# Performance work log

Hardware: AMD Instinct MI355X
Metric: run time of the kernel (lower is better)

The kernel has to match this reference:

```python
import jax, jax.numpy as jnp
import numpy as np

N, M, D = 60000, 96, 16  # voxels, centroids, descriptor_dim
NB = 4                    # batches (scenes)


def setup_inputs() -> dict:
    key = jax.random.key(0)
    ks = jax.random.split(key, 10)
    voxel_desc = jax.random.normal(ks[0], (N, D), jnp.float32)
    centroid_conf = jax.random.uniform(ks[1], (M, 1), jnp.float32)
    offsets = jax.random.normal(ks[2], (N, 3), jnp.float32)
    # 1x1 Conv2d weights act as plain linears over the channel dim
    c_in = 2 * D + 7          # 39
    c_hid = D + 3             # 19
    W1 = jax.random.normal(ks[3], (c_hid, c_in), jnp.float32) / np.sqrt(c_in)
    b1 = jax.random.normal(ks[4], (c_hid,), jnp.float32) * 0.01
    W2 = jax.random.normal(ks[5], (1, c_hid), jnp.float32) / np.sqrt(c_hid)
    b2 = jax.random.normal(ks[6], (1,), jnp.float32) * 0.01
    coords = jax.random.randint(ks[7], (N, 3), 0, 200, dtype=jnp.int32)
    batch_ids = jnp.sort(jax.random.randint(ks[8], (N,), 0, NB, dtype=jnp.int32))
    peak_indices = jnp.sort(jax.random.randint(ks[9], (M,), 0, N, dtype=jnp.int32))
    return {
        "voxel_desc": voxel_desc, "centroid_conf": centroid_conf,
        "offsets": offsets, "W1": W1, "b1": b1, "W2": W2, "b2": b2,
        "coords": coords, "batch_ids": batch_ids, "peak_indices": peak_indices,
    }


def reference(voxel_desc, centroid_conf, offsets, W1, b1, W2, b2,
              coords, batch_ids, peak_indices):
    d = voxel_desc.shape[1]
    # centroid descriptors: voxel desc at peaks + confidence  -> [M, D+1]
    cent_desc = jnp.concatenate([voxel_desc[peak_indices], centroid_conf], axis=-1)
    # voxel descriptors get offsets prepended -> [N, D+3]
    voxel_full = jnp.concatenate([offsets, voxel_desc], axis=-1)
    # distance feature (no_grad in the original): (coords + offset) - centroid coords
    new_coords = coords.astype(jnp.float32) + offsets            # [N, 3]
    cent_coords = coords[peak_indices].astype(jnp.float32)       # [M, 3]
    dists = jax.lax.stop_gradient(new_coords[:, None, :] - cent_coords[None, :, :])  # [N, M, 3]
    # 1x1 conv over channels == linear; split W1 columns to match the concat order
    # [voxel_full (D+3) | cent_desc (D+1) | dists (3)] so we never build the [N,M,2D+7] tensor
    W1v, W1c, W1d = W1[:, :d + 3], W1[:, d + 3:2 * d + 4], W1[:, 2 * d + 4:]
    pre = ((voxel_full @ W1v.T)[:, None, :]
           + (cent_desc @ W1c.T)[None, :, :]
           + jnp.einsum('nmk,hk->nmh', dists, W1d)
           + b1)                                                 # [N, M, D+3]
    h = jax.nn.relu(pre)
    logit = jnp.einsum('nmh,oh->nmo', h, W2)[..., 0] + b2[0]     # [N, M]
    logit = jnp.nan_to_num(jnp.clip(logit, -10.0, 10.0), nan=0.0)
    # pairs across different batches are -inf (never computed in the torch loop)
    same = batch_ids[:, None] == batch_ids[peak_indices][None, :]
    return jnp.where(same, logit, -jnp.inf)
```

## Files before the change

kernel.cpp:

```cpp
#include <hip/hip_runtime.h>
#include <hip/hip_bf16.h>

#define N_VOX   60000
#define M_CENT  96
#define C_IN    39
#define C_HID   19
#define RS      20
#define WSTR    40
#define TN      64
#define BLK     192


typedef const __hip_bfloat16* bfp;
__device__ __forceinline__ float bf2f(__hip_bfloat16 v) { return __bfloat162float(v); }
__device__ __forceinline__ float lo16(unsigned u) { return __uint_as_float(u << 16); }
__device__ __forceinline__ float hi16(unsigned u) { return __uint_as_float(u & 0xFFFF0000u); }
__device__ __forceinline__ unsigned bfb(float x) {
    unsigned b = __float_as_uint(x);
    return (b + 0x7FFFu + ((b >> 16) & 1u)) >> 16;
}

__global__ __launch_bounds__(BLK, 3) void fused_kernel(
    bfp voxel_desc,
    bfp centroid_conf,
    bfp offsets,
    bfp W1,
    bfp b1,
    bfp W2,
    bfp b2,
    const int* coords,
    const int* batch_ids,
    const int* peak_indices,
    __hip_bfloat16* out)
{
    __shared__ float sW[C_HID * WSTR];
    __shared__ float sB1[C_HID];
    __shared__ float sAn[TN * RS];
    __shared__ float sBm[M_CENT * RS];
    const int tid = threadIdx.x;
    const int rowbase = blockIdx.x * TN;

    for (int u = tid; u < C_HID * C_IN; u += BLK) {
        const int h = u / C_IN, k = u - h * C_IN;
        sW[h * WSTR + k] = bf2f(W1[u]);
    }
    if (tid < C_HID) sB1[tid] = bf2f(b1[tid]);

    float w2[RS];
    #pragma unroll
    for (int h = 0; h < C_HID; ++h) w2[h] = bf2f(W2[h]);
    w2[19] = 0.0f;
    const float b2f = bf2f(b2[0]);

    __syncthreads();

    const uint4* vd4 = (const uint4*)voxel_desc;

    if (tid < TN) {
        const int n = rowbase + tid;
        const int nc = (n < N_VOX) ? n : (N_VOX - 1);
        const uint4 va = vd4[nc * 2], vb = vd4[nc * 2 + 1];
        const float vd[16] = { lo16(va.x), hi16(va.x), lo16(va.y), hi16(va.y),
                               lo16(va.z), hi16(va.z), lo16(va.w), hi16(va.w),
                               lo16(vb.x), hi16(vb.x), lo16(vb.y), hi16(vb.y),
                               lo16(vb.z), hi16(vb.z), lo16(vb.w), hi16(vb.w) };
        const float o0 = bf2f(offsets[nc * 3 + 0]);
        const float o1 = bf2f(offsets[nc * 3 + 1]);
        const float o2 = bf2f(offsets[nc * 3 + 2]);
        const float nw0 = (float)coords[nc * 3 + 0] + o0;
        const float nw1 = (float)coords[nc * 3 + 1] + o1;
        const float nw2 = (float)coords[nc * 3 + 2] + o2;
        #pragma unroll 2
        for (int h = 0; h < C_HID; ++h) {
            const float4 w0 = *(const float4*)&sW[h * WSTR + 0];
            const float4 w1 = *(const float4*)&sW[h * WSTR + 4];
            const float4 w2c = *(const float4*)&sW[h * WSTR + 8];
            const float4 w3 = *(const float4*)&sW[h * WSTR + 12];
            const float4 w4 = *(const float4*)&sW[h * WSTR + 16];
            const float4 w9 = *(const float4*)&sW[h * WSTR + 36];
            float acc = sB1[h];
            acc += o0 * w0.x + o1 * w0.y + o2 * w0.z + vd[0] * w0.w;
            acc += vd[1] * w1.x + vd[2] * w1.y + vd[3] * w1.z + vd[4] * w1.w;
            acc += vd[5] * w2c.x + vd[6] * w2c.y + vd[7] * w2c.z + vd[8] * w2c.w;
            acc += vd[9] * w3.x + vd[10] * w3.y + vd[11] * w3.z + vd[12] * w3.w;
            acc += vd[13] * w4.x + vd[14] * w4.y + vd[15] * w4.z;
            acc += nw0 * w9.x + nw1 * w9.y + nw2 * w9.z;
            sAn[tid * RS + h] = acc;
        }
        sAn[tid * RS + 19] = __int_as_float(batch_ids[nc]);
    } else if (tid < TN + M_CENT) {
        const int m = tid - TN;
        const int p = peak_indices[m];
        const uint4 va = vd4[p * 2], vb = vd4[p * 2 + 1];
        const float cd[16] = { lo16(va.x), hi16(va.x), lo16(va.y), hi16(va.y),
                               lo16(va.z), hi16(va.z), lo16(va.w), hi16(va.w),
                               lo16(vb.x), hi16(vb.x), lo16(vb.y), hi16(vb.y),
                               lo16(vb.z), hi16(vb.z), lo16(vb.w), hi16(vb.w) };
        const float conf = bf2f(centroid_conf[m]);
        const float c0 = (float)coords[p * 3 + 0];
        const float c1 = (float)coords[p * 3 + 1];
        const float c2 = (float)coords[p * 3 + 2];
        #pragma unroll 2
        for (int h = 0; h < C_HID; ++h) {
            const float4 w4 = *(const float4*)&sW[h * WSTR + 16];
            const float4 w5 = *(const float4*)&sW[h * WSTR + 20];
            const float4 w6 = *(const float4*)&sW[h * WSTR + 24];
            const float4 w7 = *(const float4*)&sW[h * WSTR + 28];
            const float4 w8 = *(const float4*)&sW[h * WSTR + 32];
            const float4 w9 = *(const float4*)&sW[h * WSTR + 36];
            float acc = cd[0] * w4.w;
            acc += cd[1] * w5.x + cd[2] * w5.y + cd[3] * w5.z + cd[4] * w5.w;
            acc += cd[5] * w6.x + cd[6] * w6.y + cd[7] * w6.z + cd[8] * w6.w;
            acc += cd[9] * w7.x + cd[10] * w7.y + cd[11] * w7.z + cd[12] * w7.w;
            acc += cd[13] * w8.x + cd[14] * w8.y + cd[15] * w8.z + conf * w8.w;
            acc -= c0 * w9.x + c1 * w9.y + c2 * w9.z;
            sBm[m * RS + h] = acc;
        }
        sBm[m * RS + 19] = __int_as_float(batch_ids[p]);
    }

    __syncthreads();

    const int mp = tid % 48;
    const int q  = tid / 48;
    const int m0 = 2 * mp;

    float4 ba[5], bb[5];
    #pragma unroll
    for (int i = 0; i < 5; ++i) {
        ba[i] = *(const float4*)&sBm[m0 * RS + 4 * i];
        bb[i] = *(const float4*)&sBm[(m0 + 1) * RS + 4 * i];
    }
    const int cbA = __float_as_int(ba[4].w);
    const int cbB = __float_as_int(bb[4].w);

    #pragma unroll 4
    for (int i = 0; i < 16; ++i) {
        const int r = q + 4 * i;
        float4 an[5];
        #pragma unroll
        for (int j = 0; j < 5; ++j)
            an[j] = *(const float4*)&sAn[r * RS + 4 * j];
        const int rb = __float_as_int(an[4].w);
        float dA = 0.f, dB = 0.f;
        #pragma unroll
        for (int j = 0; j < 5; ++j) {
            dA += fmaxf(an[j].x + ba[j].x, 0.f) * w2[4 * j + 0];
            dB += fmaxf(an[j].x + bb[j].x, 0.f) * w2[4 * j + 0];
            dA += fmaxf(an[j].y + ba[j].y, 0.f) * w2[4 * j + 1];
            dB += fmaxf(an[j].y + bb[j].y, 0.f) * w2[4 * j + 1];
            dA += fmaxf(an[j].z + ba[j].z, 0.f) * w2[4 * j + 2];
            dB += fmaxf(an[j].z + bb[j].z, 0.f) * w2[4 * j + 2];
            dA += fmaxf(an[j].w + ba[j].w, 0.f) * w2[4 * j + 3];
            dB += fmaxf(an[j].w + bb[j].w, 0.f) * w2[4 * j + 3];
        }
        const float lA = dA + b2f, lB = dB + b2f;
        float cA = fminf(fmaxf(lA, -10.f), 10.f); cA = (lA == lA) ? cA : 0.f;
        float cB = fminf(fmaxf(lB, -10.f), 10.f); cB = (lB == lB) ? cB : 0.f;
        const float rA = (rb == cbA) ? cA : -10.0f;
        const float rB = (rb == cbB) ? cB : -10.0f;
        const int n = rowbase + r;
        if (n < N_VOX) {
            const unsigned pk = bfb(rA) | (bfb(rB) << 16);
            *reinterpret_cast<unsigned*>(out + (size_t)n * M_CENT + m0) = pk;
        }
    }
}

extern "C" void kernel_launch(void* const* d_in, const int* in_sizes, int n_in,
                              void* d_out, int out_size, void* d_ws, size_t ws_size,
                              hipStream_t stream) {
    bfp voxel_desc    = (bfp)d_in[0];
    bfp centroid_conf = (bfp)d_in[1];
    bfp offsets       = (bfp)d_in[2];
    bfp W1            = (bfp)d_in[3];
    bfp b1            = (bfp)d_in[4];
    bfp W2            = (bfp)d_in[5];
    bfp b2            = (bfp)d_in[6];
    const int* coords       = (const int*)d_in[7];
    const int* batch_ids    = (const int*)d_in[8];
    const int* peak_indices = (const int*)d_in[9];
    __hip_bfloat16* out = (__hip_bfloat16*)d_out;

    const int grid = (N_VOX + TN - 1) / TN;
    fused_kernel<<<grid, BLK, 0, stream>>>(
        voxel_desc, centroid_conf, offsets, W1, b1, W2, b2,
        coords, batch_ids, peak_indices, out);
}
```

Baseline: 96.94 us.

## Use packed f32x2 math with 4 centroids per thread and prefetch loads before weight staging

Each thread in the main loop now handles four centroids instead of two, with centroid rows permuted in shared memory so every row writes 8 contiguous bytes of output. The MLP inner product uses 2-wide float vectors so the compiler can emit packed FMA and max instructions. Per-thread global loads of voxel and centroid inputs are moved ahead of the weight staging and first barrier so their latency overlaps. This raises register pressure from holding four centroid rows, and the rolled loop (unroll 1) gives less instruction-level parallelism.

```diff
diff --git a/kernel.cpp b/kernel.cpp
--- a/kernel.cpp
+++ b/kernel.cpp
@@ -12,12 +12,28 @@
 
 
 typedef const __hip_bfloat16* bfp;
+typedef float f32x2 __attribute__((ext_vector_type(2)));
+
 __device__ __forceinline__ float bf2f(__hip_bfloat16 v) { return __bfloat162float(v); }
 __device__ __forceinline__ float lo16(unsigned u) { return __uint_as_float(u << 16); }
 __device__ __forceinline__ float hi16(unsigned u) { return __uint_as_float(u & 0xFFFF0000u); }
 __device__ __forceinline__ unsigned bfb(float x) {
     unsigned b = __float_as_uint(x);
     return (b + 0x7FFFu + ((b >> 16) & 1u)) >> 16;
+}
+__device__ __forceinline__ f32x2 relu2(f32x2 v, f32x2 z) {
+#if __has_builtin(__builtin_elementwise_max)
+    return __builtin_elementwise_max(v, z);
+#else
+    f32x2 r; r.x = fmaxf(v.x, 0.f); r.y = fmaxf(v.y, 0.f); return r;
+#endif
+}
+__device__ __forceinline__ f32x2 fma2(f32x2 a, f32x2 b, f32x2 c) {
+#if __has_builtin(__builtin_elementwise_fma)
+    return __builtin_elementwise_fma(a, b, c);
+#else
+    return a * b + c;
+#endif
 }
 
 __global__ __launch_bounds__(BLK, 3) void fused_kernel(
@@ -39,6 +55,33 @@
     __shared__ float sBm[M_CENT * RS];
     const int tid = threadIdx.x;
     const int rowbase = blockIdx.x * TN;
+    const uint4* vd4 = (const uint4*)voxel_desc;
+
+    uint4 va = make_uint4(0u, 0u, 0u, 0u), vb = make_uint4(0u, 0u, 0u, 0u);
+    float o0 = 0.f, o1 = 0.f, o2 = 0.f;
+    float c0 = 0.f, c1 = 0.f, c2 = 0.f, conf = 0.f;
+    int ib = 0;
+    if (tid < TN) {
+        const int n = rowbase + tid;
+        const int nc = (n < N_VOX) ? n : (N_VOX - 1);
+        va = vd4[nc * 2]; vb = vd4[nc * 2 + 1];
+        o0 = bf2f(offsets[nc * 3 + 0]);
+        o1 = bf2f(offsets[nc * 3 + 1]);
+        o2 = bf2f(offsets[nc * 3 + 2]);
+        c0 = (float)coords[nc * 3 + 0];
+        c1 = (float)coords[nc * 3 + 1];
+        c2 = (float)coords[nc * 3 + 2];
+        ib = batch_ids[nc];
+    } else if (tid < TN + M_CENT) {
+        const int m = tid - TN;
+        const int p = peak_indices[m];
+        va = vd4[p * 2]; vb = vd4[p * 2 + 1];
+        conf = bf2f(centroid_conf[m]);
+        c0 = (float)coords[p * 3 + 0];
+        c1 = (float)coords[p * 3 + 1];
+        c2 = (float)coords[p * 3 + 2];
+        ib = batch_ids[p];
+    }
 
     for (int u = tid; u < C_HID * C_IN; u += BLK) {
         const int h = u / C_IN, k = u - h * C_IN;
@@ -46,60 +89,47 @@
     }
     if (tid < C_HID) sB1[tid] = bf2f(b1[tid]);
 
-    float w2[RS];
+    f32x2 w2p[10];
     #pragma unroll
-    for (int h = 0; h < C_HID; ++h) w2[h] = bf2f(W2[h]);
-    w2[19] = 0.0f;
+    for (int j = 0; j < 10; ++j) {
+        w2p[j].x = bf2f(W2[2 * j]);
+        w2p[j].y = (2 * j + 1 < C_HID) ? bf2f(W2[2 * j + 1]) : 0.f;
+    }
     const float b2f = bf2f(b2[0]);
 
     __syncthreads();
 
-    const uint4* vd4 = (const uint4*)voxel_desc;
-
     if (tid < TN) {
-        const int n = rowbase + tid;
-        const int nc = (n < N_VOX) ? n : (N_VOX - 1);
-        const uint4 va = vd4[nc * 2], vb = vd4[nc * 2 + 1];
         const float vd[16] = { lo16(va.x), hi16(va.x), lo16(va.y), hi16(va.y),
                                lo16(va.z), hi16(va.z), lo16(va.w), hi16(va.w),
                                lo16(vb.x), hi16(vb.x), lo16(vb.y), hi16(vb.y),
                                lo16(vb.z), hi16(vb.z), lo16(vb.w), hi16(vb.w) };
-        const float o0 = bf2f(offsets[nc * 3 + 0]);
-        const float o1 = bf2f(offsets[nc * 3 + 1]);
-        const float o2 = bf2f(offsets[nc * 3 + 2]);
-        const float nw0 = (float)coords[nc * 3 + 0] + o0;
-        const float nw1 = (float)coords[nc * 3 + 1] + o1;
-        const float nw2 = (float)coords[nc * 3 + 2] + o2;
+        const float nw0 = c0 + o0, nw1 = c1 + o1, nw2 = c2 + o2;
         #pragma unroll 2
         for (int h = 0; h < C_HID; ++h) {
-            const float4 w0 = *(const float4*)&sW[h * WSTR + 0];
-            const float4 w1 = *(const float4*)&sW[h * WSTR + 4];
+            const float4 w0  = *(const float4*)&sW[h * WSTR + 0];
+            const float4 w1r = *(const float4*)&sW[h * WSTR + 4];
             const float4 w2c = *(const float4*)&sW[h * WSTR + 8];
-            const float4 w3 = *(const float4*)&sW[h * WSTR + 12];
-            const float4 w4 = *(const float4*)&sW[h * WSTR + 16];
-            const float4 w9 = *(const float4*)&sW[h * WSTR + 36];
+            const float4 w3  = *(const float4*)&sW[h * WSTR + 12];
+            const float4 w4  = *(const float4*)&sW[h * WSTR + 16];
+            const float4 w9  = *(const float4*)&sW[h * WSTR + 36];
             float acc = sB1[h];
             acc += o0 * w0.x + o1 * w0.y + o2 * w0.z + vd[0] * w0.w;
-            acc += vd[1] * w1.x + vd[2] * w1.y + vd[3] * w1.z + vd[4] * w1.w;
+            acc += vd[1] * w1r.x + vd[2] * w1r.y + vd[3] * w1r.z + vd[4] * w1r.w;
             acc += vd[5] * w2c.x + vd[6] * w2c.y + vd[7] * w2c.z + vd[8] * w2c.w;
             acc += vd[9] * w3.x + vd[10] * w3.y + vd[11] * w3.z + vd[12] * w3.w;
             acc += vd[13] * w4.x + vd[14] * w4.y + vd[15] * w4.z;
             acc += nw0 * w9.x + nw1 * w9.y + nw2 * w9.z;
             sAn[tid * RS + h] = acc;
         }
-        sAn[tid * RS + 19] = __int_as_float(batch_ids[nc]);
+        sAn[tid * RS + 19] = __int_as_float(ib);
     } else if (tid < TN + M_CENT) {
         const int m = tid - TN;
-        const int p = peak_indices[m];
-        const uint4 va = vd4[p * 2], vb = vd4[p * 2 + 1];
+        const int pr = (m & 3) * 24 + (m >> 2);
         const float cd[16] = { lo16(va.x), hi16(va.x), lo16(va.y), hi16(va.y),
                                lo16(va.z), hi16(va.z), lo16(va.w), hi16(va.w),
                                lo16(vb.x), hi16(vb.x), lo16(vb.y), hi16(vb.y),
                                lo16(vb.z), hi16(vb.z), lo16(vb.w), hi16(vb.w) };
-        const float conf = bf2f(centroid_conf[m]);
-        const float c0 = (float)coords[p * 3 + 0];
-        const float c1 = (float)coords[p * 3 + 1];
-        const float c2 = (float)coords[p * 3 + 2];
         #pragma unroll 2
         for (int h = 0; h < C_HID; ++h) {
             const float4 w4 = *(const float4*)&sW[h * WSTR + 16];
@@ -114,55 +144,66 @@
             acc += cd[9] * w7.x + cd[10] * w7.y + cd[11] * w7.z + cd[12] * w7.w;
             acc += cd[13] * w8.x + cd[14] * w8.y + cd[15] * w8.z + conf * w8.w;
             acc -= c0 * w9.x + c1 * w9.y + c2 * w9.z;
-            sBm[m * RS + h] = acc;
-        }
-        sBm[m * RS + 19] = __int_as_float(batch_ids[p]);
+            sBm[pr * RS + h] = acc;
+        }
+        sBm[pr * RS + 19] = __int_as_float(ib);
     }
 
     __syncthreads();
 
-    const int mp = tid % 48;
-    const int q  = tid / 48;
-    const int m0 = 2 * mp;
-
-    float4 ba[5], bb[5];
+    const int mg = tid % 24;
+    const int q  = tid / 24;
+
+    f32x2 bm0[10], bm1[10], bm2[10], bm3[10];
     #pragma unroll
-    for (int i = 0; i < 5; ++i) {
-        ba[i] = *(const float4*)&sBm[m0 * RS + 4 * i];
-        bb[i] = *(const float4*)&sBm[(m0 + 1) * RS + 4 * i];
-    }
-    const int cbA = __float_as_int(ba[4].w);
-    const int cbB = __float_as_int(bb[4].w);
-
-    #pragma unroll 4
-    for (int i = 0; i < 16; ++i) {
-        const int r = q + 4 * i;
-        float4 an[5];
+    for (int j = 0; j < 10; ++j) {
+        bm0[j] = *(const f32x2*)&sBm[(0 * 24 + mg) * RS + 2 * j];
+        bm1[j] = *(const f32x2*)&sBm[(1 * 24 + mg) * RS + 2 * j];
+        bm2[j] = *(const f32x2*)&sBm[(2 * 24 + mg) * RS + 2 * j];
+        bm3[j] = *(const f32x2*)&sBm[(3 * 24 + mg) * RS + 2 * j];
+    }
+    const int cb0 = __float_as_int(bm0[9].y);
+    const int cb1 = __float_as_int(bm1[9].y);
+    const int cb2 = __float_as_int(bm2[9].y);
+    const int cb3 = __float_as_int(bm3[9].y);
+    const f32x2 z2 = { 0.f, 0.f };
+
+    #pragma unroll 1
+    for (int i = 0; i < 8; ++i) {
+        const int r = q + 8 * i;
+        f32x2 an[10];
         #pragma unroll
-        for (int j = 0; j < 5; ++j)
-            an[j] = *(const float4*)&sAn[r * RS + 4 * j];
-        const int rb = __float_as_int(an[4].w);
-        float dA = 0.f, dB = 0.f;
+        for (int j = 0; j < 10; ++j)
+            an[j] = *(const f32x2*)&sAn[r * RS + 2 * j];
+        const int rb = __float_as_int(an[9].y);
+        f32x2 a0 = z2, a1 = z2, a2 = z2, a3 = z2;
         #pragma unroll
-        for (int j = 0; j < 5; ++j) {
-            dA += fmaxf(an[j].x + ba[j].x, 0.f) * w2[4 * j + 0];
-            dB += fmaxf(an[j].x + bb[j].x, 0.f) * w2[4 * j + 0];
-            dA += fmaxf(an[j].y + ba[j].y, 0.f) * w2[4 * j + 1];
-            dB += fmaxf(an[j].y + bb[j].y, 0.f) * w2[4 * j + 1];
-            dA += fmaxf(an[j].z + ba[j].z, 0.f) * w2[4 * j + 2];
-            dB += fmaxf(an[j].z + bb[j].z, 0.f) * w2[4 * j + 2];
-            dA += fmaxf(an[j].w + ba[j].w, 0.f) * w2[4 * j + 3];
-            dB += fmaxf(an[j].w + bb[j].w, 0.f) * w2[4 * j + 3];
-        }
-        const float lA = dA + b2f, lB = dB + b2f;
-        float cA = fminf(fmaxf(lA, -10.f), 10.f); cA = (lA == lA) ? cA : 0.f;
-        float cB = fminf(fmaxf(lB, -10.f), 10.f); cB = (lB == lB) ? cB : 0.f;
-        const float rA = (rb == cbA) ? cA : -10.0f;
-        const float rB = (rb == cbB) ? cB : -10.0f;
+        for (int j = 0; j < 10; ++j) {
+            const f32x2 av = an[j];
+            const f32x2 wv = w2p[j];
+            a0 = fma2(relu2(av + bm0[j], z2), wv, a0);
+            a1 = fma2(relu2(av + bm1[j], z2), wv, a1);
+            a2 = fma2(relu2(av + bm2[j], z2), wv, a2);
+            a3 = fma2(relu2(av + bm3[j], z2), wv, a3);
+        }
+        const float l0 = a0.x + a0.y + b2f;
+        const float l1 = a1.x + a1.y + b2f;
+        const float l2 = a2.x + a2.y + b2f;
+        const float l3 = a3.x + a3.y + b2f;
+        float q0 = fminf(fmaxf(l0, -10.f), 10.f); q0 = (l0 == l0) ? q0 : 0.f;
+        float q1 = fminf(fmaxf(l1, -10.f), 10.f); q1 = (l1 == l1) ? q1 : 0.f;
+        float q2 = fminf(fmaxf(l2, -10.f), 10.f); q2 = (l2 == l2) ? q2 : 0.f;
+        float q3 = fminf(fmaxf(l3, -10.f), 10.f); q3 = (l3 == l3) ? q3 : 0.f;
+        const float r0 = (rb == cb0) ? q0 : -10.0f;
+        const float r1 = (rb == cb1) ? q1 : -10.0f;
+        const float r2 = (rb == cb2) ? q2 : -10.0f;
+        const float r3 = (rb == cb3) ? q3 : -10.0f;
         const int n = rowbase + r;
         if (n < N_VOX) {
-            const unsigned pk = bfb(rA) | (bfb(rB) << 16);
-            *reinterpret_cast<unsigned*>(out + (size_t)n * M_CENT + m0) = pk;
+            const unsigned u0 = bfb(r0) | (bfb(r1) << 16);
+            const unsigned u1 = bfb(r2) | (bfb(r3) << 16);
+            *reinterpret_cast<uint2*>(out + (size_t)n * M_CENT + 4 * mg) =
+                make_uint2(u0, u1);
         }
     }
 }
```

Measured after the change: 96.23 us. No clear change (-0.7%).
